# Performance work log

Measured on AMD Instinct MI355X. Metric: run time of the kernel, lower is better.

Reference implementation:

```python
import jax, jax.numpy as jnp
import numpy as np

NUM_HEADS = 12
DIM = 768
HEAD_DIM = DIM // NUM_HEADS


def setup_inputs() -> dict:
    key = jax.random.key(0)
    k1, k2, k3, k4 = jax.random.split(key, 4)
    B, N, C = 4, 8192, DIM
    x = jax.random.normal(k1, (B, N, C), dtype=jnp.float32)
    # torch nn.Linear stores weight as (out_features, in_features)
    W_qkv = jax.random.normal(k2, (3 * C, C), dtype=jnp.float32) * (1.0 / np.sqrt(C))
    W_proj = jax.random.normal(k3, (C, C), dtype=jnp.float32) * (1.0 / np.sqrt(C))
    b_proj = jax.random.normal(k4, (C,), dtype=jnp.float32) * 0.01
    return {"x": x, "W_qkv": W_qkv, "W_proj": W_proj, "b_proj": b_proj}


def reference(x, W_qkv, W_proj, b_proj):
    B, N, C = x.shape
    H, D = NUM_HEADS, HEAD_DIM
    qkv = x @ W_qkv.T                                  # [B,N,3C]
    qkv = qkv.reshape(B, N, 3, H, D).transpose(2, 0, 3, 1, 4)  # [3,B,H,N,D]
    q, k, v = qkv[0], qkv[1], qkv[2]
    q = jax.nn.elu(q) + 1.0
    k = jax.nn.elu(k) + 1.0
    k_sum = k.sum(axis=-2)                             # [B,H,D]
    kv = jnp.einsum('bhnd,bhne->bhde', k, v)           # [B,H,D,D]
    numerator = jnp.einsum('bhnd,bhde->bhne', q, kv)   # [B,H,N,D]
    denominator = jnp.einsum('bhnd,bhd->bhn', q, k_sum)
    out = numerator / (denominator[..., None] + 1e-6)
    out = out.transpose(0, 2, 1, 3).reshape(B, N, C)   # [B,N,C]
    out = out @ W_proj.T + b_proj
    return out
```

## Files before the change

kernel.cpp:

```cpp
#include <hip/hip_runtime.h>
#include <hip/hip_bf16.h>
#include <stdint.h>

typedef __attribute__((ext_vector_type(8))) short short8;
typedef __attribute__((ext_vector_type(4))) float floatx4;

#define NB 4
#define NN 8192
#define NC 768
#define NH 12
#define ND 64
#define LDQKV 2304

__device__ __forceinline__ float bf2f(ushort u) {
    union { float f; uint32_t i; } x; x.i = ((uint32_t)u) << 16; return x.f;
}
__device__ __forceinline__ ushort f2bf(float f) {
    union { float f; uint32_t i; } x; x.f = f;
    uint32_t r = x.i + 0x7fff + ((x.i >> 16) & 1);
    return (ushort)(r >> 16);
}
typedef const __attribute__((address_space(1))) uint32_t* gas1_t;
typedef __attribute__((address_space(3))) uint32_t* las3_t;
__device__ __forceinline__ void gl_lds16(const void* g, const void* l) {
    __builtin_amdgcn_global_load_lds((gas1_t)(uintptr_t)g,
                                     (las3_t)(uint32_t)(uintptr_t)l, 16, 0, 0);
}

__global__ __launch_bounds__(256) void cvt_bf16(const float* __restrict__ src,
                                                ushort* __restrict__ dst, int n) {
    const int i = (blockIdx.x * 256 + threadIdx.x) * 8;
    if (i >= n) return;
    const float4 a = *(const float4*)(src + i);
    const float4 b = *(const float4*)(src + i + 4);
    short8 v;
    v[0] = (short)f2bf(a.x); v[1] = (short)f2bf(a.y);
    v[2] = (short)f2bf(a.z); v[3] = (short)f2bf(a.w);
    v[4] = (short)f2bf(b.x); v[5] = (short)f2bf(b.y);
    v[6] = (short)f2bf(b.z); v[7] = (short)f2bf(b.w);
    *(short8*)(dst + i) = v;
}


__device__ __forceinline__ void stage_half(const ushort* __restrict__ src, int row0,
                                           int k0, int K, ushort* dst, int t, int w) {
    const int rsub = t >> 3;
    const int ch = (t & 7) ^ (rsub & 7);
    const ushort* g0 = src + (size_t)(row0 + rsub) * K + k0 + ch * 8;
    gl_lds16(g0,                 dst + w * 512);
    gl_lds16(g0 + (size_t)64 * K, dst + 4096 + w * 512);
}

#define PHASE_SYNC() do {                                        \
    __builtin_amdgcn_s_barrier();                                \
    asm volatile("s_waitcnt lgkmcnt(0)" ::: "memory");           \
    __builtin_amdgcn_sched_barrier(0);                           \
} while (0)

template<int LDC, bool ELU, bool BIAS, typename OutT>
__global__ __launch_bounds__(512) void gemm256(const ushort* __restrict__ A,
                                               const ushort* __restrict__ Bw,
                                               const float* __restrict__ bias,
                                               OutT* __restrict__ Cout, int K) {
    __shared__ __align__(16) ushort SL[2][4][8192];
    const int t = threadIdx.x, w = t >> 6, lane = t & 63;
    const int l16 = lane & 15, quad = lane >> 4;
    const int wm = w >> 2, wn = w & 3;
    const int bro = (wn & 1) * 64;

    const int gx = gridDim.x;
    const int nwg = gx * gridDim.y;
    int bid = blockIdx.y * gx + blockIdx.x;
    bid = (bid & 7) * (nwg >> 3) + (bid >> 3);
    const int m0 = (bid / gx) * 256;
    const int n0 = (bid % gx) * 256;
    const int NT = K >> 6;

    floatx4 acc[8][4] = {};
    short8 af[4][2], b01[2][2], b23[2][2];

    stage_half(Bw, n0,       0,  K, &SL[0][0][0], t, w);
    stage_half(Bw, n0 + 128, 0,  K, &SL[0][1][0], t, w);
    stage_half(A,  m0,       0,  K, &SL[0][2][0], t, w);
    stage_half(A,  m0 + 128, 0,  K, &SL[0][3][0], t, w);
    stage_half(Bw, n0,       64, K, &SL[1][0][0], t, w);
    stage_half(Bw, n0 + 128, 64, K, &SL[1][1][0], t, w);
    asm volatile("s_waitcnt vmcnt(4)" ::: "memory");
    __builtin_amdgcn_s_barrier();

    for (int j = 0; j < NT; j++) {
        const int buf = j & 1;
        const ushort* As = &SL[buf][2 + wm][0];
        const ushort* Bs = &SL[buf][wn >> 1][0];

        #pragma unroll
        for (int mi = 0; mi < 4; mi++) {
            const int row = mi * 16 + l16;
            const int sw = (row & 7) << 3;
            const int base = row * 64 + quad * 8;
            af[mi][0] = *(const short8*)&As[base ^ sw];
            af[mi][1] = *(const short8*)&As[(base + 32) ^ sw];
        }
        #pragma unroll
        for (int ni = 0; ni < 2; ni++) {
            const int row = bro + ni * 16 + l16;
            const int sw = (row & 7) << 3;
            const int base = row * 64 + quad * 8;
            b01[ni][0] = *(const short8*)&Bs[base ^ sw];
            b01[ni][1] = *(const short8*)&Bs[(base + 32) ^ sw];
        }
        if (j + 1 < NT) stage_half(A, m0, (j + 1) * 64, K, &SL[buf ^ 1][2][0], t, w);
        asm volatile("s_waitcnt lgkmcnt(8)" ::: "memory");
        PHASE_SYNC();
        __builtin_amdgcn_s_setprio(1);
        #pragma unroll
        for (int mi = 0; mi < 4; mi++)
            #pragma unroll
            for (int ni = 0; ni < 2; ni++) {
                acc[mi][ni] = __builtin_amdgcn_mfma_f32_16x16x32_bf16(af[mi][0], b01[ni][0], acc[mi][ni], 0, 0, 0);
                acc[mi][ni] = __builtin_amdgcn_mfma_f32_16x16x32_bf16(af[mi][1], b01[ni][1], acc[mi][ni], 0, 0, 0);
            }
        __builtin_amdgcn_s_setprio(0);
        __builtin_amdgcn_s_barrier();

        #pragma unroll
        for (int ni = 0; ni < 2; ni++) {
            const int row = bro + (2 + ni) * 16 + l16;
            const int sw = (row & 7) << 3;
            const int base = row * 64 + quad * 8;
            b23[ni][0] = *(const short8*)&Bs[base ^ sw];
            b23[ni][1] = *(const short8*)&Bs[(base + 32) ^ sw];
        }
        if (j + 1 < NT) stage_half(A, m0 + 128, (j + 1) * 64, K, &SL[buf ^ 1][3][0], t, w);
        PHASE_SYNC();
        __builtin_amdgcn_s_setprio(1);
        #pragma unroll
        for (int mi = 0; mi < 4; mi++)
            #pragma unroll
            for (int ni = 0; ni < 2; ni++) {
                acc[mi][2 + ni] = __builtin_amdgcn_mfma_f32_16x16x32_bf16(af[mi][0], b23[ni][0], acc[mi][2 + ni], 0, 0, 0);
                acc[mi][2 + ni] = __builtin_amdgcn_mfma_f32_16x16x32_bf16(af[mi][1], b23[ni][1], acc[mi][2 + ni], 0, 0, 0);
            }
        __builtin_amdgcn_s_setprio(0);
        __builtin_amdgcn_s_barrier();

        #pragma unroll
        for (int mi = 0; mi < 4; mi++) {
            const int row = (4 + mi) * 16 + l16;
            const int sw = (row & 7) << 3;
            const int base = row * 64 + quad * 8;
            af[mi][0] = *(const short8*)&As[base ^ sw];
            af[mi][1] = *(const short8*)&As[(base + 32) ^ sw];
        }
        if (j + 2 < NT) stage_half(Bw, n0, (j + 2) * 64, K, &SL[buf][0][0], t, w);
        PHASE_SYNC();
        __builtin_amdgcn_s_setprio(1);
        #pragma unroll
        for (int mi = 0; mi < 4; mi++)
            #pragma unroll
            for (int ni = 0; ni < 2; ni++) {
                acc[4 + mi][ni] = __builtin_amdgcn_mfma_f32_16x16x32_bf16(af[mi][0], b01[ni][0], acc[4 + mi][ni], 0, 0, 0);
                acc[4 + mi][ni] = __builtin_amdgcn_mfma_f32_16x16x32_bf16(af[mi][1], b01[ni][1], acc[4 + mi][ni], 0, 0, 0);
            }
        __builtin_amdgcn_s_setprio(0);
        __builtin_amdgcn_s_barrier();

        if (j + 2 < NT) stage_half(Bw, n0 + 128, (j + 2) * 64, K, &SL[buf][1][0], t, w);
        __builtin_amdgcn_s_barrier();
        __builtin_amdgcn_s_setprio(1);
        #pragma unroll
        for (int mi = 0; mi < 4; mi++)
            #pragma unroll
            for (int ni = 0; ni < 2; ni++) {
                acc[4 + mi][2 + ni] = __builtin_amdgcn_mfma_f32_16x16x32_bf16(af[mi][0], b23[ni][0], acc[4 + mi][2 + ni], 0, 0, 0);
                acc[4 + mi][2 + ni] = __builtin_amdgcn_mfma_f32_16x16x32_bf16(af[mi][1], b23[ni][1], acc[4 + mi][2 + ni], 0, 0, 0);
            }
        __builtin_amdgcn_s_setprio(0);
        if (j < NT - 2) asm volatile("s_waitcnt vmcnt(4)" ::: "memory");
        else            asm volatile("s_waitcnt vmcnt(0)" ::: "memory");
        __builtin_amdgcn_s_barrier();
    }

    #pragma unroll
    for (int mi = 0; mi < 8; mi++) {
        const int row = m0 + wm * 128 + mi * 16 + quad * 4;
        #pragma unroll
        for (int n = 0; n < 4; n++) {
            const int col = n0 + wn * 64 + n * 16 + l16;
            float bval = 0.f;
            if (BIAS) bval = bias[col];
            #pragma unroll
            for (int r = 0; r < 4; r++) {
                float v = acc[mi][n][r];
                if (ELU) { if (col < 2 * NC) v = (v > 0.f) ? v + 1.f : __expf(v); }
                if (BIAS) v += bval;
                if (sizeof(OutT) == 2) Cout[(size_t)(row + r) * LDC + col] = (OutT)f2bf(v);
                else                   Cout[(size_t)(row + r) * LDC + col] = (OutT)v;
            }
        }
    }
}

template<int LDC, bool ELU, bool BIAS, typename OutT>
__global__ __launch_bounds__(256) void gemm_bt(const ushort* __restrict__ A,
                                               const ushort* __restrict__ Bw,
                                               const float* __restrict__ bias,
                                               OutT* __restrict__ Cout, int K) {
    __shared__ ushort As[128 * 32];
    __shared__ ushort Bs[128 * 32];
    const int t = threadIdx.x;
    const int w = t >> 6, lane = t & 63, l16 = lane & 15, quad = lane >> 4;
    const int wm = w & 1, wn = w >> 1;
    const int m0 = blockIdx.y * 128, n0 = blockIdx.x * 128;

    floatx4 acc[4][4] = {};

    const int rowA = t >> 2, chA = t & 3;
    const ushort* gA = A  + (size_t)(m0 + rowA) * K + chA * 8;
    const ushort* gB = Bw + (size_t)(n0 + rowA) * K + chA * 8;

    for (int k0 = 0; k0 < K; k0 += 32) {
        gl_lds16(gA + k0,                As + w * 512);
        gl_lds16(gA + k0 + 64 * K,       As + 2048 + w * 512);
        gl_lds16(gB + k0,                Bs + w * 512);
        gl_lds16(gB + k0 + 64 * K,       Bs + 2048 + w * 512);
        __syncthreads();
        short8 af[4], bfr[4];
        #pragma unroll
        for (int i = 0; i < 4; i++)
            af[i] = *(const short8*)&As[(wm * 64 + i * 16 + l16) * 32 + quad * 8];
        #pragma unroll
        for (int j = 0; j < 4; j++)
            bfr[j] = *(const short8*)&Bs[(wn * 64 + j * 16 + l16) * 32 + quad * 8];
        #pragma unroll
        for (int i = 0; i < 4; i++)
            #pragma unroll
            for (int j = 0; j < 4; j++)
                acc[i][j] = __builtin_amdgcn_mfma_f32_16x16x32_bf16(af[i], bfr[j], acc[i][j], 0, 0, 0);
        __syncthreads();
    }

    #pragma unroll
    for (int i = 0; i < 4; i++) {
        const int row = m0 + wm * 64 + i * 16 + quad * 4;
        #pragma unroll
        for (int j = 0; j < 4; j++) {
            const int col = n0 + wn * 64 + j * 16 + l16;
            float bval = 0.f;
            if (BIAS) bval = bias[col];
            #pragma unroll
            for (int r = 0; r < 4; r++) {
                float v = acc[i][j][r];
                if (ELU) { if (col < 2 * NC) v = (v > 0.f) ? v + 1.f : __expf(v); }
                if (BIAS) v += bval;
                if (sizeof(OutT) == 2) Cout[(size_t)(row + r) * LDC + col] = (OutT)f2bf(v);
                else                   Cout[(size_t)(row + r) * LDC + col] = (OutT)v;
            }
        }
    }
}

__global__ __launch_bounds__(256) void kv_ksum(const ushort* __restrict__ qkv,
                                               float* __restrict__ kv_part,
                                               float* __restrict__ ks_part) {
    __shared__ ushort kvsh[2][128 * 64];
    __shared__ float  ksred[4][64];
    ushort* klds = kvsh[0];
    ushort* vlds = kvsh[1];
    const int bh = blockIdx.y, b = bh / NH, h = bh % NH;
    const int t = threadIdx.x, w = t >> 6, lane = t & 63, l16 = lane & 15, quad = lane >> 4;
    const int n0 = blockIdx.x * 1024;
    const ushort* kbase = qkv + (size_t)(b * NN) * LDQKV + NC     + h * ND;
    const ushort* vbase = qkv + (size_t)(b * NN) * LDQKV + 2 * NC + h * ND;

    floatx4 acc[4][4] = {};
    floatx4 aks[4] = {};
    short8 bones;
    #pragma unroll
    for (int j = 0; j < 8; j++) bones[j] = (short)0x3F80;
    const int rowT = t >> 3, ch = t & 7;

    for (int s = 0; s < 8; s++) {
        const int nb = n0 + s * 128;
        #pragma unroll
        for (int i = 0; i < 4; i++) {
            const size_t r = (size_t)(nb + i * 32 + rowT) * LDQKV + ch * 8;
            gl_lds16(kbase + r, klds + i * 2048 + w * 512);
            gl_lds16(vbase + r, vlds + i * 2048 + w * 512);
        }
        __syncthreads();
        short8 af[4], bfr[4];
        #pragma unroll
        for (int dt = 0; dt < 4; dt++) {
            short8 v;
            #pragma unroll
            for (int j = 0; j < 8; j++)
                v[j] = (short)klds[(w * 32 + quad * 8 + j) * 64 + dt * 16 + l16];
            af[dt] = v;
        }
        #pragma unroll
        for (int et = 0; et < 4; et++) {
            short8 v;
            #pragma unroll
            for (int j = 0; j < 8; j++)
                v[j] = (short)vlds[(w * 32 + quad * 8 + j) * 64 + et * 16 + l16];
            bfr[et] = v;
        }
        #pragma unroll
        for (int dt = 0; dt < 4; dt++) {
            #pragma unroll
            for (int et = 0; et < 4; et++)
                acc[dt][et] = __builtin_amdgcn_mfma_f32_16x16x32_bf16(af[dt], bfr[et], acc[dt][et], 0, 0, 0);
            aks[dt] = __builtin_amdgcn_mfma_f32_16x16x32_bf16(af[dt], bones, aks[dt], 0, 0, 0);
        }
        __syncthreads();
    }

    if (l16 == 0) {
        #pragma unroll
        for (int dt = 0; dt < 4; dt++)
            #pragma unroll
            for (int r = 0; r < 4; r++)
                ksred[w][dt * 16 + quad * 4 + r] = aks[dt][r];
    }

    float* scratch = (float*)kvsh;
    if (w >= 2) {
        float* dst = scratch + (w - 2) * 4096;
        #pragma unroll
        for (int dt = 0; dt < 4; dt++)
            #pragma unroll
            for (int et = 0; et < 4; et++)
                #pragma unroll
                for (int r = 0; r < 4; r++)
                    dst[(dt * 16 + quad * 4 + r) * 64 + et * 16 + l16] = acc[dt][et][r];
    }
    __syncthreads();
    if (w < 2) {
        const float* srcp = scratch + w * 4096;
        #pragma unroll
        for (int dt = 0; dt < 4; dt++)
            #pragma unroll
            for (int et = 0; et < 4; et++)
                #pragma unroll
                for (int r = 0; r < 4; r++)
                    acc[dt][et][r] += srcp[(dt * 16 + quad * 4 + r) * 64 + et * 16 + l16];
    }
    __syncthreads();
    if (w == 1) {
        #pragma unroll
        for (int dt = 0; dt < 4; dt++)
            #pragma unroll
            for (int et = 0; et < 4; et++)
                #pragma unroll
                for (int r = 0; r < 4; r++)
                    scratch[(dt * 16 + quad * 4 + r) * 64 + et * 16 + l16] = acc[dt][et][r];
    }
    __syncthreads();
    if (w == 0) {
        float* outp = kv_part + ((size_t)blockIdx.x * 48 + bh) * 4096;
        #pragma unroll
        for (int dt = 0; dt < 4; dt++)
            #pragma unroll
            for (int et = 0; et < 4; et++)
                #pragma unroll
                for (int r = 0; r < 4; r++) {
                    const int idx = (dt * 16 + quad * 4 + r) * 64 + et * 16 + l16;
                    outp[idx] = acc[dt][et][r] + scratch[idx];
                }
    }
    if (t < 64) ks_part[(size_t)blockIdx.x * 48 * 64 + bh * 64 + t] =
        ksred[0][t] + ksred[1][t] + ksred[2][t] + ksred[3][t];
}

__global__ __launch_bounds__(256) void attn_apply(const ushort* __restrict__ qkv,
                                                  const float* __restrict__ kv_part,
                                                  const float* __restrict__ ks_part,
                                                  ushort* __restrict__ outpre) {
    __shared__ ushort kvb[64 * 80];
    const int bh = blockIdx.y, b = bh / NH, h = bh % NH;
    const int t = threadIdx.x, w = t >> 6, lane = t & 63, l16 = lane & 15, quad = lane >> 4;

    for (int i = t; i < 4096; i += 256) {
        float s = 0.f;
        #pragma unroll
        for (int c = 0; c < 8; c++) s += kv_part[((size_t)c * 48 + bh) * 4096 + i];
        kvb[(i >> 6) * 80 + (i & 63)] = f2bf(s);
    }
    for (int i = t; i < 1024; i += 256) {
        const int d = i >> 4, c = i & 15;
        float s = 0.f;
        if (c == 0) {
            #pragma unroll
            for (int cc = 0; cc < 8; cc++) s += ks_part[(size_t)cc * 48 * 64 + bh * 64 + d];
        }
        kvb[d * 80 + 64 + c] = (c == 0) ? f2bf(s) : (ushort)0;
    }
    __syncthreads();

    short8 bfr[5][2];
    #pragma unroll
    for (int et = 0; et < 5; et++)
        #pragma unroll
        for (int ks = 0; ks < 2; ks++) {
            short8 v;
            #pragma unroll
            for (int j = 0; j < 8; j++)
                v[j] = (short)kvb[(ks * 32 + quad * 8 + j) * 80 + et * 16 + l16];
            bfr[et][ks] = v;
        }

    const ushort* qbase = qkv + (size_t)(b * NN) * LDQKV + h * ND;
    ushort* obase = outpre + (size_t)(b * NN) * NC + h * ND;
    const int n0 = blockIdx.x * 1024;

    for (int it = 0; it < 16; it++) {
        const int nt = n0 + (it * 4 + w) * 16;
        const ushort* qp = qbase + (size_t)(nt + l16) * LDQKV + quad * 8;
        const short8 a0 = *(const short8*)qp;
        const short8 a1 = *(const short8*)(qp + 32);
        floatx4 acc[5] = {};
        #pragma unroll
        for (int et = 0; et < 5; et++) {
            acc[et] = __builtin_amdgcn_mfma_f32_16x16x32_bf16(a0, bfr[et][0], acc[et], 0, 0, 0);
            acc[et] = __builtin_amdgcn_mfma_f32_16x16x32_bf16(a1, bfr[et][1], acc[et], 0, 0, 0);
        }
        float dv[4];
        #pragma unroll
        for (int r = 0; r < 4; r++) dv[r] = __shfl(acc[4][r], lane & 48);
        #pragma unroll
        for (int et = 0; et < 4; et++)
            #pragma unroll
            for (int r = 0; r < 4; r++) {
                const float o = acc[et][r] / (dv[r] + 1e-6f);
                obase[(size_t)(nt + quad * 4 + r) * NC + et * 16 + l16] = f2bf(o);
            }
    }
}

extern "C" void kernel_launch(void* const* d_in, const int* in_sizes, int n_in,
                              void* d_out, int out_size, void* d_ws, size_t ws_size,
                              hipStream_t stream) {
    (void)in_sizes; (void)n_in; (void)out_size; (void)ws_size;
    const float* X     = (const float*)d_in[0];
    const float* Wqkv  = (const float*)d_in[1];
    const float* Wproj = (const float*)d_in[2];
    const float* bproj = (const float*)d_in[3];
    float* out = (float*)d_out;

    char* ws = (char*)d_ws;
    size_t off = 0;
    ushort* qkv     = (ushort*)(ws + off); off += (size_t)32768 * 2304 * 2;
    ushort* outpre  = (ushort*)(ws + off); off += (size_t)32768 * 768 * 2;
    ushort* xbf     = (ushort*)(ws + off); off += (size_t)32768 * 768 * 2;
    ushort* wqkvbf  = (ushort*)(ws + off); off += (size_t)2304 * 768 * 2;
    ushort* wprojbf = (ushort*)(ws + off);
    float* kv_part = (float*)xbf;
    float* ks_part = kv_part + (size_t)8 * 48 * 4096;

    const int nx = 32768 * 768, nwq = 2304 * 768, nwp = 768 * 768;
    cvt_bf16<<<nx  / (256 * 8), 256, 0, stream>>>(X,     xbf,     nx);
    cvt_bf16<<<nwq / (256 * 8), 256, 0, stream>>>(Wqkv,  wqkvbf,  nwq);
    cvt_bf16<<<nwp / (256 * 8), 256, 0, stream>>>(Wproj, wprojbf, nwp);

    gemm256<LDQKV, true, false, ushort><<<dim3(9, 128), 512, 0, stream>>>(xbf, wqkvbf, nullptr, qkv, NC);
    kv_ksum<<<dim3(8, 48), 256, 0, stream>>>(qkv, kv_part, ks_part);
    attn_apply<<<dim3(8, 48), 256, 0, stream>>>(qkv, kv_part, ks_part, outpre);
    gemm_bt<NC, false, true, float><<<dim3(6, 256), 256, 0, stream>>>(outpre, wprojbf, bproj, out, NC);
}
```

Measured before the change: 441.5 us.

## Prefetch GEMM A tiles two steps ahead and double-buffer kv_ksum loads

In the GEMM main loop, A-tile global-to-LDS staging now runs two K-steps ahead alongside the B tiles instead of one step ahead mid-iteration, with the vmcnt waits adjusted to match. The kv_ksum kernel gets a double-buffered LDS ping-pong so the next 128-row chunk of K/V loads while the current one is computed. Both changes aim to hide global memory latency behind MFMA work. The cost is doubled LDS in kv_ksum, which may reduce occupancy, and more outstanding loads in flight. The hand-counted waitcnt values must also stay correct.

```diff
diff --git a/kernel.cpp b/kernel.cpp
--- a/kernel.cpp
+++ b/kernel.cpp
@@ -85,7 +85,9 @@
     stage_half(A,  m0 + 128, 0,  K, &SL[0][3][0], t, w);
     stage_half(Bw, n0,       64, K, &SL[1][0][0], t, w);
     stage_half(Bw, n0 + 128, 64, K, &SL[1][1][0], t, w);
-    asm volatile("s_waitcnt vmcnt(4)" ::: "memory");
+    stage_half(A,  m0,       64, K, &SL[1][2][0], t, w);
+    stage_half(A,  m0 + 128, 64, K, &SL[1][3][0], t, w);
+    asm volatile("s_waitcnt vmcnt(8)" ::: "memory");
     __builtin_amdgcn_s_barrier();
 
     for (int j = 0; j < NT; j++) {
@@ -109,7 +111,6 @@
             b01[ni][0] = *(const short8*)&Bs[base ^ sw];
             b01[ni][1] = *(const short8*)&Bs[(base + 32) ^ sw];
         }
-        if (j + 1 < NT) stage_half(A, m0, (j + 1) * 64, K, &SL[buf ^ 1][2][0], t, w);
         asm volatile("s_waitcnt lgkmcnt(8)" ::: "memory");
         PHASE_SYNC();
         __builtin_amdgcn_s_setprio(1);
@@ -131,7 +132,6 @@
             b23[ni][0] = *(const short8*)&Bs[base ^ sw];
             b23[ni][1] = *(const short8*)&Bs[(base + 32) ^ sw];
         }
-        if (j + 1 < NT) stage_half(A, m0 + 128, (j + 1) * 64, K, &SL[buf ^ 1][3][0], t, w);
         PHASE_SYNC();
         __builtin_amdgcn_s_setprio(1);
         #pragma unroll
@@ -165,7 +165,11 @@
         __builtin_amdgcn_s_setprio(0);
         __builtin_amdgcn_s_barrier();
 
-        if (j + 2 < NT) stage_half(Bw, n0 + 128, (j + 2) * 64, K, &SL[buf][1][0], t, w);
+        if (j + 2 < NT) {
+            stage_half(Bw, n0 + 128, (j + 2) * 64, K, &SL[buf][1][0], t, w);
+            stage_half(A,  m0,       (j + 2) * 64, K, &SL[buf][2][0], t, w);
+            stage_half(A,  m0 + 128, (j + 2) * 64, K, &SL[buf][3][0], t, w);
+        }
         __builtin_amdgcn_s_barrier();
         __builtin_amdgcn_s_setprio(1);
         #pragma unroll
@@ -176,7 +180,7 @@
                 acc[4 + mi][2 + ni] = __builtin_amdgcn_mfma_f32_16x16x32_bf16(af[mi][1], b23[ni][1], acc[4 + mi][2 + ni], 0, 0, 0);
             }
         __builtin_amdgcn_s_setprio(0);
-        if (j < NT - 2) asm volatile("s_waitcnt vmcnt(4)" ::: "memory");
+        if (j < NT - 2) asm volatile("s_waitcnt vmcnt(8)" ::: "memory");
         else            asm volatile("s_waitcnt vmcnt(0)" ::: "memory");
         __builtin_amdgcn_s_barrier();
     }
@@ -263,10 +267,8 @@
 __global__ __launch_bounds__(256) void kv_ksum(const ushort* __restrict__ qkv,
                                                float* __restrict__ kv_part,
                                                float* __restrict__ ks_part) {
-    __shared__ ushort kvsh[2][128 * 64];
+    __shared__ ushort kvsh[2][2][128 * 64];
     __shared__ float  ksred[4][64];
-    ushort* klds = kvsh[0];
-    ushort* vlds = kvsh[1];
     const int bh = blockIdx.y, b = bh / NH, h = bh % NH;
     const int t = threadIdx.x, w = t >> 6, lane = t & 63, l16 = lane & 15, quad = lane >> 4;
     const int n0 = blockIdx.x * 1024;
@@ -280,15 +282,24 @@
     for (int j = 0; j < 8; j++) bones[j] = (short)0x3F80;
     const int rowT = t >> 3, ch = t & 7;
 
+    #define KV_STAGE(s) do {                                                  \
+        const int nb_ = n0 + (s) * 128;                                       \
+        _Pragma("unroll")                                                     \
+        for (int i_ = 0; i_ < 4; i_++) {                                      \
+            const size_t r_ = (size_t)(nb_ + i_ * 32 + rowT) * LDQKV + ch * 8;\
+            gl_lds16(kbase + r_, &kvsh[(s) & 1][0][0] + i_ * 2048 + w * 512); \
+            gl_lds16(vbase + r_, &kvsh[(s) & 1][1][0] + i_ * 2048 + w * 512); \
+        }                                                                     \
+    } while (0)
+
+    KV_STAGE(0);
     for (int s = 0; s < 8; s++) {
-        const int nb = n0 + s * 128;
-        #pragma unroll
-        for (int i = 0; i < 4; i++) {
-            const size_t r = (size_t)(nb + i * 32 + rowT) * LDQKV + ch * 8;
-            gl_lds16(kbase + r, klds + i * 2048 + w * 512);
-            gl_lds16(vbase + r, vlds + i * 2048 + w * 512);
-        }
-        __syncthreads();
+        if (s < 7) KV_STAGE(s + 1);
+        if (s < 7) asm volatile("s_waitcnt vmcnt(8)" ::: "memory");
+        else       asm volatile("s_waitcnt vmcnt(0)" ::: "memory");
+        __builtin_amdgcn_s_barrier();
+        const ushort* klds = &kvsh[s & 1][0][0];
+        const ushort* vlds = &kvsh[s & 1][1][0];
         short8 af[4], bfr[4];
         #pragma unroll
         for (int dt = 0; dt < 4; dt++) {
@@ -313,8 +324,9 @@
                 acc[dt][et] = __builtin_amdgcn_mfma_f32_16x16x32_bf16(af[dt], bfr[et], acc[dt][et], 0, 0, 0);
             aks[dt] = __builtin_amdgcn_mfma_f32_16x16x32_bf16(af[dt], bones, aks[dt], 0, 0, 0);
         }
-        __syncthreads();
-    }
+        __builtin_amdgcn_s_barrier();
+    }
+    #undef KV_STAGE
 
     if (l16 == 0) {
         #pragma unroll
```

Measured after the change: 452.4 us. 1.02x slower.
